# Kernel tuning notes

Hardware: AMD Instinct MI355X
Metric: run time of the kernel (lower is better)

Reference implementation:

```python
import jax, jax.numpy as jnp
import numpy as np

HIDDEN = 2048
NUM_OPS = 3
BATCH = 16384


def setup_inputs() -> dict:
    key = jax.random.key(0)
    ks = jax.random.split(key, 6)
    x = jax.random.normal(ks[0], (BATCH, HIDDEN), dtype=jnp.float32)
    chosen_ops = jax.random.randint(ks[1], (BATCH,), 0, NUM_OPS, dtype=jnp.int32)
    # Stacked expert params; torch nn.Linear computes x @ W.T + b, W: [out, in].
    # We store W already transposed to [in, out] for direct einsum.
    scale = 1.0 / np.sqrt(HIDDEN)
    W1 = jax.random.uniform(ks[2], (NUM_OPS, HIDDEN, HIDDEN), jnp.float32, -scale, scale)
    b1 = jax.random.uniform(ks[3], (NUM_OPS, HIDDEN), jnp.float32, -scale, scale)
    W2 = jax.random.uniform(ks[4], (NUM_OPS, HIDDEN, HIDDEN), jnp.float32, -scale, scale)
    b2 = jax.random.uniform(ks[5], (NUM_OPS, HIDDEN), jnp.float32, -scale, scale)
    return {"x": x, "W1": W1, "b1": b1, "W2": W2, "b2": b2, "chosen_ops": chosen_ops}


def reference(x, W1, b1, W2, b2, chosen_ops):
    # Temper.apply_operators: each row of x is routed to one expert MLP:
    #   out[i] = relu(W2_e @ relu(W1_e @ x[i] + b1_e) + b2_e), e = chosen_ops[i]
    # operator_freshness starts at zeros, so the +0.01*result branch is inactive.
    # Vectorized: run all experts on all rows (small fixed NUM_OPS), then select.
    h = jax.nn.relu(jnp.einsum('bh,ehk->ebk', x, W1) + b1[:, None, :])   # [E,B,H]
    y = jax.nn.relu(jnp.einsum('ebh,ehk->ebk', h, W2) + b2[:, None, :])  # [E,B,H]
    out = y[chosen_ops, jnp.arange(x.shape[0]), :]                        # [B,H]
    return out
```

## Files before the change

kernel.cpp:

```cpp
#include <hip/hip_runtime.h>
#include <hip/hip_bf16.h>
#include <stdint.h>

#define HIDDEN 2048
#define BATCH 16384
#define NUM_OPS 3
#define NT_M 67
#define M_CAP (NT_M * 256)
#define NXT 16
#define KT 32

typedef __attribute__((ext_vector_type(4))) float f32x4;
typedef __attribute__((ext_vector_type(8))) short short8;
typedef __attribute__((ext_vector_type(8))) __bf16 bf16x8;

static constexpr size_t XB_SZ   = (size_t)M_CAP * HIDDEN * 2;
static constexpr size_t H_SZ    = XB_SZ;
static constexpr size_t WT_SZ   = (size_t)NUM_OPS * HIDDEN * HIDDEN * 2;
static constexpr size_t PERM_SZ = (size_t)M_CAP * 4;

__device__ __forceinline__ unsigned f2bf(float f) {
  unsigned u = __float_as_uint(f);
  return (u + 0x7FFFu + ((u >> 16) & 1u)) >> 16;
}

__device__ __forceinline__ void async_ld16(const void* g, void* l) {
  __builtin_amdgcn_global_load_lds(
      (__attribute__((address_space(1))) void*)(void*)g,
      (__attribute__((address_space(3))) void*)l, 16, 0, 0);
}

__global__ __launch_bounds__(256) void k_count(const int* __restrict__ ops,
                                               int* __restrict__ cnt,
                                               int* __restrict__ perm) {
  int i = blockIdx.x * 256 + threadIdx.x;
  if (i < M_CAP) perm[i] = -1;
  int e = (i < BATCH) ? ops[i] : -1;
  int lane = threadIdx.x & 63;
#pragma unroll
  for (int ee = 0; ee < NUM_OPS; ee++) {
    unsigned long long m = __ballot(e == ee);
    if (lane == 0 && m) atomicAdd(&cnt[ee], __popcll(m));
  }
}

__global__ void k_scan(const int* __restrict__ cnt, int* __restrict__ seg,
                       int* __restrict__ te) {
  int a0 = (cnt[0] + 255) & ~255;
  int a1 = (cnt[1] + 255) & ~255;
  int a2 = (cnt[2] + 255) & ~255;
  if (threadIdx.x == 0) {
    seg[0] = 0; seg[1] = a0; seg[2] = a0 + a1; seg[3] = a0 + a1 + a2;
  }
  for (int t = threadIdx.x; t < NT_M; t += 64) {
    int row = t * 256;
    int ex = -1;
    if (row < a0) ex = 0;
    else if (row < a0 + a1) ex = 1;
    else if (row < a0 + a1 + a2) ex = 2;
    te[t] = ex;
  }
}

__global__ __launch_bounds__(256) void k_perm(const int* __restrict__ ops,
                                              const int* __restrict__ seg,
                                              int* __restrict__ c2,
                                              int* __restrict__ perm) {
  int b = blockIdx.x * 256 + threadIdx.x;
  int e = (b < BATCH) ? ops[b] : -1;
  int lane = threadIdx.x & 63;
#pragma unroll
  for (int ee = 0; ee < NUM_OPS; ee++) {
    unsigned long long m = __ballot(e == ee);
    if (m) {
      int base = 0;
      if (lane == 0) base = atomicAdd(&c2[ee], __popcll(m));
      base = __shfl(base, 0);
      if (e == ee) {
        int myoff = __popcll(m & ((1ull << lane) - 1ull));
        perm[seg[ee] + base + myoff] = b;
      }
    }
  }
}

__global__ __launch_bounds__(256) void k_prep(const float* __restrict__ x,
                                              const int* __restrict__ perm,
                                              short* __restrict__ xb,
                                              const float* __restrict__ W1,
                                              const float* __restrict__ W2,
                                              short* __restrict__ W1t,
                                              short* __restrict__ W2t) {
  int tid = threadIdx.x;
  if (blockIdx.x < M_CAP) {
    int pos = blockIdx.x;
    int b = perm[pos];
    uint4 o;
    if (b < 0) {
      o = make_uint4(0u, 0u, 0u, 0u);
    } else {
      const float4* xs = (const float4*)(x + (size_t)b * HIDDEN + tid * 8);
      float4 f0 = xs[0], f1 = xs[1];
      o.x = f2bf(f0.x) | (f2bf(f0.y) << 16);
      o.y = f2bf(f0.z) | (f2bf(f0.w) << 16);
      o.z = f2bf(f1.x) | (f2bf(f1.y) << 16);
      o.w = f2bf(f1.z) | (f2bf(f1.w) << 16);
    }
    *(uint4*)(xb + (size_t)pos * HIDDEN + tid * 8) = o;
  } else {
    __shared__ float t[64][65];
    int q = blockIdx.x - M_CAP;
    int z = q >> 10;
    int rem = q & 1023;
    int by = rem >> 5, bx = rem & 31;
    const float* src = (z < 3) ? (W1 + (size_t)z * HIDDEN * HIDDEN)
                               : (W2 + (size_t)(z - 3) * HIDDEN * HIDDEN);
    short* dst = (z < 3) ? (W1t + (size_t)z * HIDDEN * HIDDEN)
                         : (W2t + (size_t)(z - 3) * HIDDEN * HIDDEN);
    int k0 = by * 64;
    int n0 = bx * 64;
    {
      int kk = tid >> 4, n4 = (tid & 15) * 4;
#pragma unroll
      for (int p = 0; p < 4; p++) {
        int k = p * 16 + kk;
        *(float4*)&t[k][n4] = *(const float4*)&src[(size_t)(k0 + k) * HIDDEN + n0 + n4];
      }
    }
    __syncthreads();
#pragma unroll
    for (int p = 0; p < 2; p++) {
      int qq = p * 256 + tid;
      int n = qq >> 3, uc = qq & 7;
      uint4 o;
      unsigned* po = (unsigned*)&o;
#pragma unroll
      for (int j = 0; j < 4; j++) {
        float a = t[uc * 8 + 2 * j][n];
        float c = t[uc * 8 + 2 * j + 1][n];
        po[j] = f2bf(a) | (f2bf(c) << 16);
      }
      *(uint4*)&dst[(size_t)(n0 + n) * HIDDEN + k0 + uc * 8] = o;
    }
  }
}

template <int SECOND>
__global__ __launch_bounds__(512, 2)
void gemm256(const short* __restrict__ A, const short* __restrict__ Wt,
             const float* __restrict__ bias, const int* __restrict__ te,
             const int* __restrict__ perm, short* __restrict__ Hout,
             float* __restrict__ Yout) {
  extern __shared__ short lds[];

  const int lin = blockIdx.x;
  const int xt = lin & 15;
  const int yt = lin >> 4;
  const int e = te[yt];
  if (e < 0) return;

  const int tid = threadIdx.x;
  const int wid = tid >> 6;
  const int lane = tid & 63;
  const int quad = lane >> 4;
  const int l16 = lane & 15;
  const int wm64 = (wid >> 1) * 64;
  const int bn64 = (wid & 1) * 64;

  const short* Ag = A + (size_t)yt * 256 * HIDDEN;
  const short* Bg = Wt + (size_t)e * HIDDEN * HIDDEN + (size_t)xt * 128 * HIDDEN;

  const int r0 = tid >> 3;
  const int c0 = ((tid & 7) ^ (r0 & 7)) * 8;
  const short* pA = Ag + (size_t)r0 * HIDDEN + c0;
  const short* pB = Bg + (size_t)r0 * HIDDEN + c0;
  const int dstw = wid * 512;

  auto stageA01 = [&](int sb, int k0) {
    async_ld16(pA + k0,                lds + sb + dstw);
    async_ld16(pA + 64 * HIDDEN + k0,  lds + sb + 4096 + dstw);
  };
  auto stageA23 = [&](int sb, int k0) {
    async_ld16(pA + 128 * HIDDEN + k0, lds + sb + 8192 + dstw);
    async_ld16(pA + 192 * HIDDEN + k0, lds + sb + 12288 + dstw);
  };
  auto stageB0 = [&](int sb, int k0) {
    async_ld16(pB + k0,                lds + sb + 16384 + dstw);
  };
  auto stageB1 = [&](int sb, int k0) {
    async_ld16(pB + 64 * HIDDEN + k0,  lds + sb + 20480 + dstw);
  };
  auto frag = [&](int base, int r, int q) {
    return __builtin_bit_cast(bf16x8,
        *(const short8*)(lds + base + r * 64 + ((q ^ (r & 7)) * 8)));
  };

  f32x4 acc[4][4] = {};
  bf16x8 af[4], bfr[4];

  int cur = 0, nxt = 24576, stg = 49152;

  stageA01(cur, 0); stageA23(cur, 0); stageB0(cur, 0); stageB1(cur, 0);
  stageA01(nxt, 64); stageA23(nxt, 64); stageB0(nxt, 64); stageB1(nxt, 64);
  asm volatile("s_waitcnt vmcnt(6)" ::: "memory");
  __builtin_amdgcn_s_barrier();

  for (int t = 0; t < KT; ++t) {
    const int k2 = (t + 2) * 64;
    const bool pf = (t + 2 < KT);

#pragma unroll
    for (int i = 0; i < 4; ++i) af[i]  = frag(cur,        wm64 + i * 16 + l16, quad);
#pragma unroll
    for (int j = 0; j < 4; ++j) bfr[j] = frag(cur + 16384, bn64 + j * 16 + l16, quad);
    if (pf) { stageA01(stg, k2); stageB0(stg, k2); }
    __builtin_amdgcn_sched_barrier(0);
    __builtin_amdgcn_s_barrier();
    asm volatile("s_waitcnt lgkmcnt(0)" ::: "memory");
    __builtin_amdgcn_sched_barrier(0);
    __builtin_amdgcn_s_setprio(1);
#pragma unroll
    for (int i = 0; i < 4; ++i)
#pragma unroll
      for (int j = 0; j < 4; ++j)
        acc[i][j] = __builtin_amdgcn_mfma_f32_16x16x32_bf16(af[i], bfr[j], acc[i][j], 0, 0, 0);
    __builtin_amdgcn_s_setprio(0);
    __builtin_amdgcn_sched_barrier(0);
    __builtin_amdgcn_s_barrier();

#pragma unroll
    for (int i = 0; i < 4; ++i) af[i]  = frag(cur,        wm64 + i * 16 + l16, 4 + quad);
#pragma unroll
    for (int j = 0; j < 4; ++j) bfr[j] = frag(cur + 16384, bn64 + j * 16 + l16, 4 + quad);
    if (pf) { stageA23(stg, k2); stageB1(stg, k2); }
    __builtin_amdgcn_sched_barrier(0);
    __builtin_amdgcn_s_barrier();
    asm volatile("s_waitcnt lgkmcnt(0)" ::: "memory");
    __builtin_amdgcn_sched_barrier(0);
    __builtin_amdgcn_s_setprio(1);
#pragma unroll
    for (int i = 0; i < 4; ++i)
#pragma unroll
      for (int j = 0; j < 4; ++j)
        acc[i][j] = __builtin_amdgcn_mfma_f32_16x16x32_bf16(af[i], bfr[j], acc[i][j], 0, 0, 0);
    __builtin_amdgcn_s_setprio(0);
    __builtin_amdgcn_sched_barrier(0);
    if (pf) asm volatile("s_waitcnt vmcnt(6)" ::: "memory");
    else    asm volatile("s_waitcnt vmcnt(0)" ::: "memory");
    __builtin_amdgcn_s_barrier();

    int tmp = cur; cur = nxt; nxt = stg; stg = tmp;
  }

  const int rb = yt * 256 + wm64 + quad * 4;
  const int cb = xt * 128 + bn64 + l16;
#pragma unroll
  for (int i = 0; i < 4; ++i) {
#pragma unroll
    for (int r = 0; r < 4; ++r) {
      const int m = rb + i * 16 + r;
      int bidx = 0;
      if (SECOND) bidx = perm[m];
#pragma unroll
      for (int j = 0; j < 4; ++j) {
        const int n = cb + j * 16;
        float v = acc[i][j][r] + bias[e * HIDDEN + n];
        v = v > 0.0f ? v : 0.0f;
        if (SECOND) {
          if (bidx >= 0) Yout[(size_t)bidx * HIDDEN + n] = v;
        } else {
          Hout[(size_t)m * HIDDEN + n] = (short)f2bf(v);
        }
      }
    }
  }
}

extern "C" void kernel_launch(void* const* d_in, const int* in_sizes, int n_in,
                              void* d_out, int out_size, void* d_ws, size_t ws_size,
                              hipStream_t stream) {
  const float* x  = (const float*)d_in[0];
  const float* W1 = (const float*)d_in[1];
  const float* b1 = (const float*)d_in[2];
  const float* W2 = (const float*)d_in[3];
  const float* b2 = (const float*)d_in[4];
  const int* ops  = (const int*)d_in[5];
  float* out = (float*)d_out;

  char* ws = (char*)d_ws;
  short* xb  = (short*)(ws);
  short* h   = (short*)(ws + XB_SZ);
  short* w1t = (short*)(ws + XB_SZ + H_SZ);
  short* w2t = (short*)(ws + XB_SZ + H_SZ + WT_SZ);
  int* perm  = (int*)(ws + XB_SZ + H_SZ + 2 * WT_SZ);
  int* meta  = (int*)(ws + XB_SZ + H_SZ + 2 * WT_SZ + PERM_SZ);
  int* cnt = meta;
  int* c2  = meta + 4;
  int* seg = meta + 8;
  int* te  = meta + 16;

  static bool attr_done = false;
  if (!attr_done) {
    hipFuncSetAttribute((const void*)gemm256<0>,
                        hipFuncAttributeMaxDynamicSharedMemorySize, 147456);
    hipFuncSetAttribute((const void*)gemm256<1>,
                        hipFuncAttributeMaxDynamicSharedMemorySize, 147456);
    attr_done = true;
  }

  hipMemsetAsync(meta, 0, 32, stream);
  k_count<<<(M_CAP + 255) / 256, 256, 0, stream>>>(ops, cnt, perm);
  k_scan<<<1, 64, 0, stream>>>(cnt, seg, te);
  k_perm<<<BATCH / 256, 256, 0, stream>>>(ops, seg, c2, perm);
  k_prep<<<M_CAP + 6 * 32 * 32, 256, 0, stream>>>(x, perm, xb, W1, W2, w1t, w2t);
  gemm256<0><<<NXT * NT_M, 512, 147456, stream>>>(xb, w1t, b1, te, perm, h, nullptr);
  gemm256<1><<<NXT * NT_M, 512, 147456, stream>>>(h, w2t, b2, te, perm, nullptr, out);
}
```

Measured before the change: 677.1 us.

## Load B fragments directly from global memory and double-buffer only A in LDS

The GEMM kernel no longer stages the weight (B) tile through LDS. Each wave loads its B MFMA fragments straight from global memory into registers, and only the A tile is double-buffered in LDS. The triple-buffered pipeline with fine-grained barriers and priority hints becomes a simpler two-buffer loop with __syncthreads, and LDS use drops from 144KB to 64KB. This removes LDS traffic for B and may allow more blocks per CU. The cost is that global-load latency for B is no longer hidden by prefetching, and B data is duplicated across waves that share columns.

```diff
diff --git a/kernel.cpp b/kernel.cpp
--- a/kernel.cpp
+++ b/kernel.cpp
@@ -146,8 +146,8 @@
 }
 
 template <int SECOND>
-__global__ __launch_bounds__(512, 2)
-void gemm256(const short* __restrict__ A, const short* __restrict__ Wt,
+__global__ __launch_bounds__(512)
+void gemm_bd(const short* __restrict__ A, const short* __restrict__ Wt,
              const float* __restrict__ bias, const int* __restrict__ te,
              const int* __restrict__ perm, short* __restrict__ Hout,
              float* __restrict__ Yout) {
@@ -173,83 +173,56 @@
   const int r0 = tid >> 3;
   const int c0 = ((tid & 7) ^ (r0 & 7)) * 8;
   const short* pA = Ag + (size_t)r0 * HIDDEN + c0;
-  const short* pB = Bg + (size_t)r0 * HIDDEN + c0;
   const int dstw = wid * 512;
 
-  auto stageA01 = [&](int sb, int k0) {
+  auto stageA = [&](int sb, int k0) {
     async_ld16(pA + k0,                lds + sb + dstw);
     async_ld16(pA + 64 * HIDDEN + k0,  lds + sb + 4096 + dstw);
-  };
-  auto stageA23 = [&](int sb, int k0) {
     async_ld16(pA + 128 * HIDDEN + k0, lds + sb + 8192 + dstw);
     async_ld16(pA + 192 * HIDDEN + k0, lds + sb + 12288 + dstw);
-  };
-  auto stageB0 = [&](int sb, int k0) {
-    async_ld16(pB + k0,                lds + sb + 16384 + dstw);
-  };
-  auto stageB1 = [&](int sb, int k0) {
-    async_ld16(pB + 64 * HIDDEN + k0,  lds + sb + 20480 + dstw);
   };
   auto frag = [&](int base, int r, int q) {
     return __builtin_bit_cast(bf16x8,
         *(const short8*)(lds + base + r * 64 + ((q ^ (r & 7)) * 8)));
   };
 
+  const short* pB = Bg + (size_t)(bn64 + l16) * HIDDEN + quad * 8;
+
   f32x4 acc[4][4] = {};
-  bf16x8 af[4], bfr[4];
-
-  int cur = 0, nxt = 24576, stg = 49152;
-
-  stageA01(cur, 0); stageA23(cur, 0); stageB0(cur, 0); stageB1(cur, 0);
-  stageA01(nxt, 64); stageA23(nxt, 64); stageB0(nxt, 64); stageB1(nxt, 64);
-  asm volatile("s_waitcnt vmcnt(6)" ::: "memory");
-  __builtin_amdgcn_s_barrier();
+  int cur = 0, nxt = 16384;
+
+  stageA(cur, 0);
+  __syncthreads();
 
   for (int t = 0; t < KT; ++t) {
-    const int k2 = (t + 2) * 64;
-    const bool pf = (t + 2 < KT);
-
-#pragma unroll
-    for (int i = 0; i < 4; ++i) af[i]  = frag(cur,        wm64 + i * 16 + l16, quad);
-#pragma unroll
-    for (int j = 0; j < 4; ++j) bfr[j] = frag(cur + 16384, bn64 + j * 16 + l16, quad);
-    if (pf) { stageA01(stg, k2); stageB0(stg, k2); }
-    __builtin_amdgcn_sched_barrier(0);
-    __builtin_amdgcn_s_barrier();
-    asm volatile("s_waitcnt lgkmcnt(0)" ::: "memory");
-    __builtin_amdgcn_sched_barrier(0);
-    __builtin_amdgcn_s_setprio(1);
+    const int k0 = t * 64;
+    bf16x8 b0[4], b1[4];
+#pragma unroll
+    for (int j = 0; j < 4; ++j) {
+      const short* pj = pB + (size_t)j * 16 * HIDDEN + k0;
+      b0[j] = __builtin_bit_cast(bf16x8, *(const short8*)(pj));
+      b1[j] = __builtin_bit_cast(bf16x8, *(const short8*)(pj + 32));
+    }
+    if (t + 1 < KT) stageA(nxt, k0 + 64);
+
+    bf16x8 af[4];
+#pragma unroll
+    for (int i = 0; i < 4; ++i) af[i] = frag(cur, wm64 + i * 16 + l16, quad);
 #pragma unroll
     for (int i = 0; i < 4; ++i)
 #pragma unroll
       for (int j = 0; j < 4; ++j)
-        acc[i][j] = __builtin_amdgcn_mfma_f32_16x16x32_bf16(af[i], bfr[j], acc[i][j], 0, 0, 0);
-    __builtin_amdgcn_s_setprio(0);
-    __builtin_amdgcn_sched_barrier(0);
-    __builtin_amdgcn_s_barrier();
-
-#pragma unroll
-    for (int i = 0; i < 4; ++i) af[i]  = frag(cur,        wm64 + i * 16 + l16, 4 + quad);
-#pragma unroll
-    for (int j = 0; j < 4; ++j) bfr[j] = frag(cur + 16384, bn64 + j * 16 + l16, 4 + quad);
-    if (pf) { stageA23(stg, k2); stageB1(stg, k2); }
-    __builtin_amdgcn_sched_barrier(0);
-    __builtin_amdgcn_s_barrier();
-    asm volatile("s_waitcnt lgkmcnt(0)" ::: "memory");
-    __builtin_amdgcn_sched_barrier(0);
-    __builtin_amdgcn_s_setprio(1);
+        acc[i][j] = __builtin_amdgcn_mfma_f32_16x16x32_bf16(af[i], b0[j], acc[i][j], 0, 0, 0);
+#pragma unroll
+    for (int i = 0; i < 4; ++i) af[i] = frag(cur, wm64 + i * 16 + l16, 4 + quad);
 #pragma unroll
     for (int i = 0; i < 4; ++i)
 #pragma unroll
       for (int j = 0; j < 4; ++j)
-        acc[i][j] = __builtin_amdgcn_mfma_f32_16x16x32_bf16(af[i], bfr[j], acc[i][j], 0, 0, 0);
-    __builtin_amdgcn_s_setprio(0);
-    __builtin_amdgcn_sched_barrier(0);
-    if (pf) asm volatile("s_waitcnt vmcnt(6)" ::: "memory");
-    else    asm volatile("s_waitcnt vmcnt(0)" ::: "memory");
-    __builtin_amdgcn_s_barrier();
-
-    int tmp = cur; cur = nxt; nxt = stg; stg = tmp;
+        acc[i][j] = __builtin_amdgcn_mfma_f32_16x16x32_bf16(af[i], b1[j], acc[i][j], 0, 0, 0);
+
+    __syncthreads();
+    int tmp = cur; cur = nxt; nxt = tmp;
   }
 
   const int rb = yt * 256 + wm64 + quad * 4;
@@ -301,10 +274,10 @@
 
   static bool attr_done = false;
   if (!attr_done) {
-    hipFuncSetAttribute((const void*)gemm256<0>,
-                        hipFuncAttributeMaxDynamicSharedMemorySize, 147456);
-    hipFuncSetAttribute((const void*)gemm256<1>,
-                        hipFuncAttributeMaxDynamicSharedMemorySize, 147456);
+    hipFuncSetAttribute((const void*)gemm_bd<0>,
+                        hipFuncAttributeMaxDynamicSharedMemorySize, 65536);
+    hipFuncSetAttribute((const void*)gemm_bd<1>,
+                        hipFuncAttributeMaxDynamicSharedMemorySize, 65536);
     attr_done = true;
   }
 
@@ -313,6 +286,6 @@
   k_scan<<<1, 64, 0, stream>>>(cnt, seg, te);
   k_perm<<<BATCH / 256, 256, 0, stream>>>(ops, seg, c2, perm);
   k_prep<<<M_CAP + 6 * 32 * 32, 256, 0, stream>>>(x, perm, xb, W1, W2, w1t, w2t);
-  gemm256<0><<<NXT * NT_M, 512, 147456, stream>>>(xb, w1t, b1, te, perm, h, nullptr);
-  gemm256<1><<<NXT * NT_M, 512, 147456, stream>>>(h, w2t, b2, te, perm, nullptr, out);
-}
+  gemm_bd<0><<<NXT * NT_M, 512, 65536, stream>>>(xb, w1t, b1, te, perm, h, nullptr);
+  gemm_bd<1><<<NXT * NT_M, 512, 65536, stream>>>(h, w2t, b2, te, perm, nullptr, out);
+}
```

After: 991.2 us. 46.4% more time.
